# Kernel optimization log

Hardware: AMD Instinct MI355X
Metric: run time of the kernel (lower is better)

The kernel has to match this reference:

```python
import math
import jax, jax.numpy as jnp
import numpy as np

NUM_HEADS = 16
BASE = 10000.0


def _rope_sin_cos(seq_len, head_dim):
    # theta_j = pos / base^(2j/dim), j in [0, dim//2)
    j = jnp.arange(head_dim // 2, dtype=jnp.float32)
    inv_freq = jnp.power(jnp.float32(BASE), -2.0 * j / head_dim)  # [d/2]
    pos = jnp.arange(seq_len, dtype=jnp.float32)
    ang = pos[:, None] * inv_freq[None, :]          # [S, d/2]
    sin, cos = jnp.sin(ang), jnp.cos(ang)
    # interleave-repeat each entry twice: [S, d]
    sin2 = jnp.stack([sin, sin], axis=-1).reshape(seq_len, head_dim)
    cos2 = jnp.stack([cos, cos], axis=-1).reshape(seq_len, head_dim)
    return sin2, cos2


def _apply_rope(x, sin2, cos2):
    # x: [B, H, S, d]; rotate-half interleaved: (-x1, x0, -x3, x2, ...)
    x_even, x_odd = x[..., 0::2], x[..., 1::2]
    rot = jnp.stack([-x_odd, x_even], axis=-1).reshape(x.shape)
    return x * cos2 + rot * sin2


def setup_inputs() -> dict:
    key = jax.random.key(0)
    ks = jax.random.split(key, 9)
    B, S, H = 2, 2048, 2048
    sc = 1.0 / math.sqrt(H)
    return {
        "hidden_state": jax.random.normal(ks[0], (B, S, H), jnp.float32),
        "Wq": jax.random.normal(ks[1], (H, H), jnp.float32) * sc,
        "bq": jax.random.normal(ks[2], (H,), jnp.float32) * 0.01,
        "Wk": jax.random.normal(ks[3], (H, H), jnp.float32) * sc,
        "bk": jax.random.normal(ks[4], (H,), jnp.float32) * 0.01,
        "Wv": jax.random.normal(ks[5], (H, H), jnp.float32) * sc,
        "bv": jax.random.normal(ks[6], (H,), jnp.float32) * 0.01,
        "Wo": jax.random.normal(ks[7], (H, H), jnp.float32) * sc,
        "bo": jax.random.normal(ks[8], (H,), jnp.float32) * 0.01,
    }


def reference(hidden_state, Wq, bq, Wk, bk, Wv, bv, Wo, bo):
    B, S, H = hidden_state.shape
    nh = NUM_HEADS
    hd = H // nh

    def proj(W, b):
        y = jnp.einsum('bsh,hd->bsd', hidden_state, W) + b
        return y.reshape(B, S, nh, hd).transpose(0, 2, 1, 3)  # [B,nh,S,hd]

    q = proj(Wq, bq)
    k = proj(Wk, bk)
    v = proj(Wv, bv)

    sin2, cos2 = _rope_sin_cos(S, hd)  # [S, hd]
    q = _apply_rope(q, sin2, cos2)
    k = _apply_rope(k, sin2, cos2)

    scale = 1.0 / math.sqrt(hd)
    attn = jnp.einsum('bhqd,bhkd->bhqk', q, k) * scale  # [B,nh,S,S]
    attn = jax.nn.softmax(attn, axis=-1)
    out = jnp.einsum('bhqk,bhkd->bhqd', attn, v)
    out = out.transpose(0, 2, 1, 3).reshape(B, S, H)
    return jnp.einsum('bsh,hd->bsd', out, Wo) + bo
```

## Files before the change

### kernel.cpp

```cpp
#include <hip/hip_runtime.h>
#include <math.h>


typedef __bf16 bf16;
typedef __attribute__((ext_vector_type(8))) __bf16 bf16x8;
typedef __attribute__((ext_vector_type(4))) __bf16 bf16x4;
typedef __attribute__((ext_vector_type(4))) float f32x4;

#define S_LEN 2048
#define NHEAD 16
#define HD 128

__device__ __forceinline__ f32x4 mfma16(bf16x8 a, bf16x8 b, f32x4 c) {
    return __builtin_amdgcn_mfma_f32_16x16x32_bf16(a, b, c, 0, 0, 0);
}

__device__ __forceinline__ void gload16(const bf16* g, bf16* s) {
    __builtin_amdgcn_global_load_lds(
        (const __attribute__((address_space(1))) void*)g,
        (__attribute__((address_space(3))) void*)s, 16, 0, 0);
}

__global__ __launch_bounds__(256) void transpose_cvt(const float* __restrict__ W,
                                                     bf16* __restrict__ Wt,
                                                     int Kd, int Nd) {
    __shared__ float tile[32][33];
    const int tx = threadIdx.x & 31, ty = threadIdx.x >> 5;
    const int bn = blockIdx.x * 32, bk = blockIdx.y * 32;
#pragma unroll
    for (int r = 0; r < 32; r += 8)
        tile[ty + r][tx] = W[(size_t)(bk + ty + r) * Nd + bn + tx];
    __syncthreads();
#pragma unroll
    for (int r = 0; r < 32; r += 8)
        Wt[(size_t)(bn + ty + r) * Kd + bk + tx] = (bf16)tile[tx][ty + r];
}

__global__ __launch_bounds__(256)
void prep(const float* __restrict__ Wq, const float* __restrict__ Wk,
          const float* __restrict__ Wv, const float* __restrict__ Wo,
          bf16* __restrict__ Wt3, bf16* __restrict__ WoT,
          const float* __restrict__ hs, bf16* __restrict__ Xb,
          float* __restrict__ stab, float* __restrict__ ctab) {
    const int z = blockIdx.z;
    const int id = blockIdx.y * 64 + blockIdx.x;
    const int t = threadIdx.x;
    if (z == 4) {
        const int g = id * 256 + t;
        if (g < 262144) {
            const int s = g >> 7, d = g & 127;
            const float invf = exp2f(-0.20762050593046013f * (float)(d >> 1));
            float sn, cs;
            sincosf((float)s * invf, &sn, &cs);
            stab[g] = sn;
            ctab[g] = cs;
        }
        return;
    }
    if (z == 5) {
        const size_t i = ((size_t)id * 256 + t) * 8;
        const float4 v0 = *(const float4*)(hs + i);
        const float4 v1 = *(const float4*)(hs + i + 4);
        bf16x8 o;
        o[0] = (bf16)v0.x; o[1] = (bf16)v0.y; o[2] = (bf16)v0.z; o[3] = (bf16)v0.w;
        o[4] = (bf16)v1.x; o[5] = (bf16)v1.y; o[6] = (bf16)v1.z; o[7] = (bf16)v1.w;
        *(bf16x8*)(Xb + i) = o;
        return;
    }
    __shared__ float tile[32][33];
    const float* W = (z == 0) ? Wq : (z == 1) ? Wk : (z == 2) ? Wv : Wo;
    bf16* Wt = (z < 3) ? (Wt3 + (size_t)z * 2048 * 2048) : WoT;
    const int tx = t & 31, ty = t >> 5;
    const int bn = blockIdx.x * 32, bk = blockIdx.y * 32;
#pragma unroll
    for (int r = 0; r < 32; r += 8)
        tile[ty + r][tx] = W[(size_t)(bk + ty + r) * 2048 + bn + tx];
    __syncthreads();
#pragma unroll
    for (int r = 0; r < 32; r += 8)
        Wt[(size_t)(bn + ty + r) * 2048 + bk + tx] = (bf16)tile[tx][ty + r];
}

__global__ __launch_bounds__(256, 3)
void gemm_qkv(const bf16* __restrict__ A, const bf16* __restrict__ Bt,
              const float* __restrict__ bq, const float* __restrict__ bk,
              const float* __restrict__ bv, bf16* __restrict__ Qo,
              bf16* __restrict__ Ko, bf16* __restrict__ Vo,
              const float* __restrict__ stab, const float* __restrict__ ctab) {
    const int K = 2048;
    __shared__ __align__(16) bf16 smem[17408];
    bf16* As = smem;
    bf16* Bs = smem + 8192;
    const int t = threadIdx.x;
    const int w = t >> 6, l = t & 63;
    const int lr = l & 15, lq = l >> 4;
    const int m0 = blockIdx.y * 128, n0 = blockIdx.x * 128;
    const int wm = (w >> 1) * 64, wn = (w & 1) * 64;
    const int seg = n0 >> 11;
    const float* bias = (seg == 0) ? bq : (seg == 1) ? bk : bv;
    bf16* outB = (seg == 0) ? Qo : (seg == 1) ? Ko : Vo;

    f32x4 acc[4][4];
    const f32x4 fz = {0.f, 0.f, 0.f, 0.f};
#pragma unroll
    for (int i = 0; i < 4; ++i)
#pragma unroll
        for (int j = 0; j < 4; ++j) acc[i][j] = fz;

    const bf16* aG[4];
    const bf16* bG[4];
    bf16* aL[4];
    bf16* bL[4];
#pragma unroll
    for (int c = 0; c < 4; ++c) {
        const int ch = c * 256 + t;
        const int row = ch >> 3, ccp = ch & 7;
        const int cc = ccp ^ (row & 7);
        aG[c] = &A[(size_t)(m0 + row) * K + cc * 8];
        bG[c] = &Bt[(size_t)(n0 + row) * K + cc * 8];
        aL[c] = &As[ch * 8];
        bL[c] = &Bs[ch * 8];
    }

    for (int k0 = 0; k0 < K; k0 += 64) {
#pragma unroll
        for (int c = 0; c < 4; ++c) {
            gload16(aG[c] + k0, aL[c]);
            gload16(bG[c] + k0, bL[c]);
        }
        __syncthreads();
#pragma unroll
        for (int s = 0; s < 2; ++s) {
            bf16x8 af[4], bfr[4];
#pragma unroll
            for (int i = 0; i < 4; ++i) {
                const int row = wm + i * 16 + lr;
                af[i] = *(const bf16x8*)&As[(row * 8 + ((s * 4 + lq) ^ (row & 7))) * 8];
            }
#pragma unroll
            for (int j = 0; j < 4; ++j) {
                const int row = wn + j * 16 + lr;
                bfr[j] = *(const bf16x8*)&Bs[(row * 8 + ((s * 4 + lq) ^ (row & 7))) * 8];
            }
#pragma unroll
            for (int i = 0; i < 4; ++i)
#pragma unroll
                for (int j = 0; j < 4; ++j)
                    acc[i][j] = mfma16(af[i], bfr[j], acc[i][j]);
        }
        __syncthreads();
    }

    if (seg == 2) {
#pragma unroll
        for (int i = 0; i < 4; ++i) {
            const int rl0 = wm + i * 16 + lq * 4;
#pragma unroll
            for (int j = 0; j < 4; ++j) {
                const int cl = wn + j * 16 + lr;
                const float bv_ = bias[(n0 & 2047) + cl];
#pragma unroll
                for (int r = 0; r < 4; ++r)
                    smem[cl * 136 + rl0 + r] = (bf16)(acc[i][j][r] + bv_);
            }
        }
        __syncthreads();
        const int b = m0 >> 11;
#pragma unroll
        for (int p = 0; p < 8; ++p) {
            const int idx = p * 256 + t;
            const int col = idx >> 4, ch = idx & 15;
            const bf16x8 v = *(const bf16x8*)&smem[col * 136 + ch * 8];
            const int cg2 = (n0 & 2047) + col;
            const int h = cg2 >> 7, d = cg2 & 127;
            *(bf16x8*)&outB[((size_t)((b << 4) | h) * HD + d) * S_LEN +
                            (m0 & 2047) + ch * 8] = v;
        }
    } else {
#pragma unroll
        for (int i = 0; i < 4; ++i) {
            const int rg0 = m0 + wm + i * 16 + lq * 4;
#pragma unroll
            for (int j = 0; j < 4; ++j) {
                const int cg2 = (n0 & 2047) + wn + j * 16 + lr;
                const float bv_ = bias[cg2];
                const int h = cg2 >> 7, d = cg2 & 127;
#pragma unroll
                for (int r = 0; r < 4; ++r) {
                    const int rg = rg0 + r;
                    const int b = rg >> 11, s = rg & 2047;
                    float v = acc[i][j][r] + bv_;
                    float p = __shfl_xor(v, 1);
                    const float sn = stab[(s << 7) | d];
                    const float cs = ctab[(s << 7) | d];
                    float o = (d & 1) ? (v * cs + p * sn) : (v * cs - p * sn);
                    if (seg == 0) o *= 0.08838834764831843f;
                    outB[((size_t)((b << 4) + h) * S_LEN + s) * HD + d] = (bf16)o;
                }
            }
        }
    }
}

__global__ __launch_bounds__(256, 3)
void gemm_out(const bf16* __restrict__ A, const bf16* __restrict__ Bt,
              const float* __restrict__ bias, float* __restrict__ outF,
              int M, int N, int K) {
    __shared__ __align__(16) bf16 As[128 * 64];
    __shared__ __align__(16) bf16 Bs[128 * 64];
    const int t = threadIdx.x;
    const int w = t >> 6, l = t & 63;
    const int lr = l & 15, lq = l >> 4;
    const int m0 = blockIdx.y * 128, n0 = blockIdx.x * 128;
    const int wm = (w >> 1) * 64, wn = (w & 1) * 64;

    f32x4 acc[4][4];
    const f32x4 fz = {0.f, 0.f, 0.f, 0.f};
#pragma unroll
    for (int i = 0; i < 4; ++i)
#pragma unroll
        for (int j = 0; j < 4; ++j) acc[i][j] = fz;

    const bf16* aG[4];
    const bf16* bG[4];
    bf16* aL[4];
    bf16* bL[4];
#pragma unroll
    for (int c = 0; c < 4; ++c) {
        const int ch = c * 256 + t;
        const int row = ch >> 3, ccp = ch & 7;
        const int cc = ccp ^ (row & 7);
        aG[c] = &A[(size_t)(m0 + row) * K + cc * 8];
        bG[c] = &Bt[(size_t)(n0 + row) * K + cc * 8];
        aL[c] = &As[ch * 8];
        bL[c] = &Bs[ch * 8];
    }

    for (int k0 = 0; k0 < K; k0 += 64) {
#pragma unroll
        for (int c = 0; c < 4; ++c) {
            gload16(aG[c] + k0, aL[c]);
            gload16(bG[c] + k0, bL[c]);
        }
        __syncthreads();
#pragma unroll
        for (int s = 0; s < 2; ++s) {
            bf16x8 af[4], bfr[4];
#pragma unroll
            for (int i = 0; i < 4; ++i) {
                const int row = wm + i * 16 + lr;
                af[i] = *(const bf16x8*)&As[(row * 8 + ((s * 4 + lq) ^ (row & 7))) * 8];
            }
#pragma unroll
            for (int j = 0; j < 4; ++j) {
                const int row = wn + j * 16 + lr;
                bfr[j] = *(const bf16x8*)&Bs[(row * 8 + ((s * 4 + lq) ^ (row & 7))) * 8];
            }
#pragma unroll
            for (int i = 0; i < 4; ++i)
#pragma unroll
                for (int j = 0; j < 4; ++j)
                    acc[i][j] = mfma16(af[i], bfr[j], acc[i][j]);
        }
        __syncthreads();
    }
#pragma unroll
    for (int i = 0; i < 4; ++i) {
        const int rg0 = m0 + wm + i * 16 + lq * 4;
#pragma unroll
        for (int j = 0; j < 4; ++j) {
            const int cg = n0 + wn + j * 16 + lr;
            const float bv = bias[cg];
#pragma unroll
            for (int r = 0; r < 4; ++r)
                outF[(size_t)(rg0 + r) * N + cg] = acc[i][j][r] + bv;
        }
    }
}

__global__ __launch_bounds__(256, 2)
void attn_fwd(const bf16* __restrict__ Q, const bf16* __restrict__ K,
              const bf16* __restrict__ Vt, bf16* __restrict__ AO) {
    __shared__ __align__(16) bf16 Ks[64 * 128];
    __shared__ __align__(16) bf16 Vs[128 * 64];
    __shared__ __align__(16) bf16 Ps[128 * 64];
    const int t = threadIdx.x;
    const int w = t >> 6, l = t & 63;
    const int lr = l & 15, lq = l >> 4;
    const int blk = blockIdx.x;
    const int qt = (blk >> 3) & 15;
    const int bh = ((blk & 7) << 2) | (blk >> 7);
    const int b = bh >> 4, h = bh & 15;

    const bf16* Qp = Q + (size_t)bh * S_LEN * HD;
    const bf16* Kp = K + (size_t)bh * S_LEN * HD;
    const bf16* Vp = Vt + (size_t)bh * HD * S_LEN;

    bf16x8 qf[2][4];
#pragma unroll
    for (int i = 0; i < 2; ++i)
#pragma unroll
        for (int s = 0; s < 4; ++s)
            qf[i][s] = *(const bf16x8*)&Qp[(size_t)(qt * 128 + w * 32 + i * 16 + lr) * HD +
                                           s * 32 + lq * 8];

    f32x4 O[2][8];
    const f32x4 fz = {0.f, 0.f, 0.f, 0.f};
#pragma unroll
    for (int i = 0; i < 2; ++i)
#pragma unroll
        for (int jd = 0; jd < 8; ++jd) O[i][jd] = fz;
    float lst[2][4] = {{0.f, 0.f, 0.f, 0.f}, {0.f, 0.f, 0.f, 0.f}};

    bf16x8 rK[4], rV[4];
#pragma unroll
    for (int c = 0; c < 4; ++c) {
        const int chunk = c * 256 + t;
        const int kr = chunk >> 4, kc = chunk & 15;
        const int vr = chunk >> 3, vc = chunk & 7;
        rK[c] = *(const bf16x8*)&Kp[(size_t)kr * HD + kc * 8];
        rV[c] = *(const bf16x8*)&Vp[(size_t)vr * S_LEN + vc * 8];
    }

    for (int kt = 0; kt < 32; ++kt) {
#pragma unroll
        for (int c = 0; c < 4; ++c) {
            const int chunk = c * 256 + t;
            const int kr = chunk >> 4, kc = chunk & 15;
            const int vr = chunk >> 3, vc = chunk & 7;
            *(bf16x8*)&Ks[(kr * 16 + (kc ^ (kr & 15))) * 8] = rK[c];
            *(bf16x8*)&Vs[(vr * 8 + (vc ^ (vr & 7))) * 8] = rV[c];
        }
        __syncthreads();

        if (kt < 31) {
#pragma unroll
            for (int c = 0; c < 4; ++c) {
                const int chunk = c * 256 + t;
                const int kr = chunk >> 4, kc = chunk & 15;
                const int vr = chunk >> 3, vc = chunk & 7;
                rK[c] = *(const bf16x8*)&Kp[(size_t)((kt + 1) * 64 + kr) * HD + kc * 8];
                rV[c] = *(const bf16x8*)&Vp[(size_t)vr * S_LEN + (kt + 1) * 64 + vc * 8];
            }
        }

        f32x4 Sc[2][4];
#pragma unroll
        for (int i = 0; i < 2; ++i)
#pragma unroll
            for (int j = 0; j < 4; ++j) Sc[i][j] = fz;
#pragma unroll
        for (int s = 0; s < 4; ++s) {
            bf16x8 kf[4];
#pragma unroll
            for (int j = 0; j < 4; ++j) {
                const int krow = j * 16 + lr;
                kf[j] = *(const bf16x8*)&Ks[(krow * 16 + ((s * 4 + lq) ^ (krow & 15))) * 8];
            }
            __builtin_amdgcn_s_setprio(1);
#pragma unroll
            for (int i = 0; i < 2; ++i)
#pragma unroll
                for (int j = 0; j < 4; ++j)
                    Sc[i][j] = mfma16(qf[i][s], kf[j], Sc[i][j]);
            __builtin_amdgcn_s_setprio(0);
        }

#pragma unroll
        for (int i = 0; i < 2; ++i)
#pragma unroll
            for (int j = 0; j < 4; ++j)
#pragma unroll
                for (int r = 0; r < 4; ++r) {
                    const float p = __expf(Sc[i][j][r]);
                    lst[i][r] += p;
                    const int prow = w * 32 + i * 16 + lq * 4 + r;
                    const int pch = (j * 2 + (lr >> 3)) ^ (prow & 7);
                    Ps[(prow * 8 + pch) * 8 + (lr & 7)] = (bf16)p;
                }

#pragma unroll
        for (int s = 0; s < 2; ++s) {
            bf16x8 pf[2], vf[8];
#pragma unroll
            for (int i = 0; i < 2; ++i) {
                const int prow = w * 32 + i * 16 + lr;
                pf[i] = *(const bf16x8*)&Ps[(prow * 8 + ((s * 4 + lq) ^ (prow & 7))) * 8];
            }
#pragma unroll
            for (int jd = 0; jd < 8; ++jd) {
                const int vrow = jd * 16 + lr;
                vf[jd] = *(const bf16x8*)&Vs[(vrow * 8 + ((s * 4 + lq) ^ (vrow & 7))) * 8];
            }
            __builtin_amdgcn_s_setprio(1);
#pragma unroll
            for (int i = 0; i < 2; ++i)
#pragma unroll
                for (int jd = 0; jd < 8; ++jd)
                    O[i][jd] = mfma16(pf[i], vf[jd], O[i][jd]);
            __builtin_amdgcn_s_setprio(0);
        }
        __syncthreads();
    }

#pragma unroll
    for (int mask = 1; mask < 16; mask <<= 1)
#pragma unroll
        for (int i = 0; i < 2; ++i)
#pragma unroll
            for (int r = 0; r < 4; ++r) lst[i][r] += __shfl_xor(lst[i][r], mask);

#pragma unroll
    for (int i = 0; i < 2; ++i)
#pragma unroll
        for (int jd = 0; jd < 8; ++jd)
#pragma unroll
            for (int r = 0; r < 4; ++r) {
                const int srow = qt * 128 + w * 32 + i * 16 + lq * 4 + r;
                const float v = O[i][jd][r] / lst[i][r];
                AO[(size_t)(b * S_LEN + srow) * 2048 + h * HD + jd * 16 + lr] = (bf16)v;
            }
}

extern "C" void kernel_launch(void* const* d_in, const int* in_sizes, int n_in,
                              void* d_out, int out_size, void* d_ws, size_t ws_size,
                              hipStream_t stream) {
    const float* hs = (const float*)d_in[0];
    const float* Wq = (const float*)d_in[1];
    const float* bq = (const float*)d_in[2];
    const float* Wk = (const float*)d_in[3];
    const float* bk = (const float*)d_in[4];
    const float* Wv = (const float*)d_in[5];
    const float* bv = (const float*)d_in[6];
    const float* Wo = (const float*)d_in[7];
    const float* bo = (const float*)d_in[8];
    float* out = (float*)d_out;

    char* ws = (char*)d_ws;
    bf16* Xb = (bf16*)ws;
    bf16* Wt3 = (bf16*)(ws + (size_t)16777216);
    bf16* Qb = (bf16*)(ws + (size_t)41943040);
    bf16* Kb = (bf16*)(ws + (size_t)58720256);
    bf16* Vb = (bf16*)(ws + (size_t)75497472);
    float* stab = (float*)(ws + (size_t)92274688);
    float* ctab = (float*)(ws + (size_t)93323264);
    bf16* AO = Xb;

    const bool bigws = ws_size >= (size_t)102760448;
    bf16* WoT = bigws ? (bf16*)(ws + (size_t)94371840) : Wt3;

    if (bigws) {
        prep<<<dim3(64, 64, 6), 256, 0, stream>>>(Wq, Wk, Wv, Wo, Wt3, WoT,
                                                  hs, Xb, stab, ctab);
    } else {
        prep<<<dim3(64, 64, 5), 256, 0, stream>>>(Wq, Wk, Wv, Wq, Wt3, WoT,
                                                  hs, Xb, stab, ctab);
    }
    gemm_qkv<<<dim3(48, 32), 256, 0, stream>>>(Xb, Wt3, bq, bk, bv, Qb, Kb, Vb,
                                               stab, ctab);
    attn_fwd<<<512, 256, 0, stream>>>(Qb, Kb, Vb, AO);
    if (!bigws)
        transpose_cvt<<<dim3(64, 64), 256, 0, stream>>>(Wo, Wt3, 2048, 2048);
    gemm_out<<<dim3(16, 32), 256, 0, stream>>>(AO, WoT, bo, out, 4096, 2048, 2048);
}
```

Baseline: 391.5 us.

## Swap load strategies between output GEMM and attention K/V staging

The output-projection GEMM changes from direct global-to-LDS loads to register-staged prefetching, which fetches the next K tile into registers while the current tile is computed. The attention kernel goes the other way: its register-prefetched K/V tiles become direct global_load_lds transfers with the XOR swizzle applied on the global address side. The GEMM gains overlap of loads with MFMA work at the cost of extra registers. The attention kernel saves registers and VALU work but loses the software prefetch overlap.

```diff
diff --git a/kernel.cpp b/kernel.cpp
--- a/kernel.cpp
+++ b/kernel.cpp
@@ -221,28 +221,34 @@
 #pragma unroll
         for (int j = 0; j < 4; ++j) acc[i][j] = fz;
 
-    const bf16* aG[4];
-    const bf16* bG[4];
-    bf16* aL[4];
-    bf16* bL[4];
+    bf16x8 rA[4], rB[4];
 #pragma unroll
     for (int c = 0; c < 4; ++c) {
-        const int ch = c * 256 + t;
-        const int row = ch >> 3, ccp = ch & 7;
-        const int cc = ccp ^ (row & 7);
-        aG[c] = &A[(size_t)(m0 + row) * K + cc * 8];
-        bG[c] = &Bt[(size_t)(n0 + row) * K + cc * 8];
-        aL[c] = &As[ch * 8];
-        bL[c] = &Bs[ch * 8];
+        const int chunk = c * 256 + t;
+        const int row = chunk >> 3, cc = chunk & 7;
+        rA[c] = *(const bf16x8*)&A[(size_t)(m0 + row) * K + cc * 8];
+        rB[c] = *(const bf16x8*)&Bt[(size_t)(n0 + row) * K + cc * 8];
     }
 
     for (int k0 = 0; k0 < K; k0 += 64) {
 #pragma unroll
         for (int c = 0; c < 4; ++c) {
-            gload16(aG[c] + k0, aL[c]);
-            gload16(bG[c] + k0, bL[c]);
-        }
-        __syncthreads();
+            const int chunk = c * 256 + t;
+            const int row = chunk >> 3, cc = chunk & 7;
+            const int d = (row * 8 + (cc ^ (row & 7))) * 8;
+            *(bf16x8*)&As[d] = rA[c];
+            *(bf16x8*)&Bs[d] = rB[c];
+        }
+        __syncthreads();
+        if (k0 + 64 < K) {
+#pragma unroll
+            for (int c = 0; c < 4; ++c) {
+                const int chunk = c * 256 + t;
+                const int row = chunk >> 3, cc = chunk & 7;
+                rA[c] = *(const bf16x8*)&A[(size_t)(m0 + row) * K + k0 + 64 + cc * 8];
+                rB[c] = *(const bf16x8*)&Bt[(size_t)(n0 + row) * K + k0 + 64 + cc * 8];
+            }
+        }
 #pragma unroll
         for (int s = 0; s < 2; ++s) {
             bf16x8 af[4], bfr[4];
@@ -312,37 +318,28 @@
         for (int jd = 0; jd < 8; ++jd) O[i][jd] = fz;
     float lst[2][4] = {{0.f, 0.f, 0.f, 0.f}, {0.f, 0.f, 0.f, 0.f}};
 
-    bf16x8 rK[4], rV[4];
+    const bf16* kG[4];
+    const bf16* vG[4];
+    bf16* kL[4];
+    bf16* vL[4];
 #pragma unroll
     for (int c = 0; c < 4; ++c) {
-        const int chunk = c * 256 + t;
-        const int kr = chunk >> 4, kc = chunk & 15;
-        const int vr = chunk >> 3, vc = chunk & 7;
-        rK[c] = *(const bf16x8*)&Kp[(size_t)kr * HD + kc * 8];
-        rV[c] = *(const bf16x8*)&Vp[(size_t)vr * S_LEN + vc * 8];
+        const int ch = c * 256 + t;
+        const int kr = ch >> 4, kc = ch & 15;
+        const int vr = ch >> 3, vc = ch & 7;
+        kG[c] = &Kp[(size_t)kr * HD + (kc ^ (kr & 15)) * 8];
+        vG[c] = &Vp[(size_t)vr * S_LEN + (vc ^ (vr & 7)) * 8];
+        kL[c] = &Ks[ch * 8];
+        vL[c] = &Vs[ch * 8];
     }
 
     for (int kt = 0; kt < 32; ++kt) {
 #pragma unroll
         for (int c = 0; c < 4; ++c) {
-            const int chunk = c * 256 + t;
-            const int kr = chunk >> 4, kc = chunk & 15;
-            const int vr = chunk >> 3, vc = chunk & 7;
-            *(bf16x8*)&Ks[(kr * 16 + (kc ^ (kr & 15))) * 8] = rK[c];
-            *(bf16x8*)&Vs[(vr * 8 + (vc ^ (vr & 7))) * 8] = rV[c];
-        }
-        __syncthreads();
-
-        if (kt < 31) {
-#pragma unroll
-            for (int c = 0; c < 4; ++c) {
-                const int chunk = c * 256 + t;
-                const int kr = chunk >> 4, kc = chunk & 15;
-                const int vr = chunk >> 3, vc = chunk & 7;
-                rK[c] = *(const bf16x8*)&Kp[(size_t)((kt + 1) * 64 + kr) * HD + kc * 8];
-                rV[c] = *(const bf16x8*)&Vp[(size_t)vr * S_LEN + (kt + 1) * 64 + vc * 8];
-            }
-        }
+            gload16(kG[c] + (size_t)kt * 64 * HD, kL[c]);
+            gload16(vG[c] + kt * 64, vL[c]);
+        }
+        __syncthreads();
 
         f32x4 Sc[2][4];
 #pragma unroll
```

Result: faster. 378.7 us (-3.3%).
